# Performance work log

Hardware: AMD Instinct MI355X
Metric: run time of the kernel (lower is better)

The kernel has to match this reference:

```python
import jax, jax.numpy as jnp
import numpy as np

B, S, E, H = 4, 2048, 1024, 16
DH = E // H  # 64
DF = 4 * E   # 4096
EPS = 1e-5


def layer_norm(x, g, b):
    mu = jnp.mean(x, axis=-1, keepdims=True)
    var = jnp.mean(jnp.square(x - mu), axis=-1, keepdims=True)
    return (x - mu) * jax.lax.rsqrt(var + EPS) * g + b


def setup_inputs() -> dict:
    key = jax.random.key(0)
    ks = jax.random.split(key, 16)
    s_e = 1.0 / np.sqrt(E)
    s_f = 1.0 / np.sqrt(DF)
    inp = {
        "x": jax.random.normal(ks[0], (B, S, E), jnp.float32),
        # per-head projections stacked over heads: [H, E, DH]
        "wq": jax.random.normal(ks[1], (H, E, DH), jnp.float32) * s_e,
        "wk": jax.random.normal(ks[2], (H, E, DH), jnp.float32) * s_e,
        "wv": jax.random.normal(ks[3], (H, E, DH), jnp.float32) * s_e,
        # output projection [H*DH, E] with bias
        "wo": jax.random.normal(ks[4], (H * DH, E), jnp.float32) * s_e,
        "bo": jax.random.normal(ks[5], (E,), jnp.float32) * 0.01,
        # SwiGLU FFN
        "w1": jax.random.normal(ks[6], (E, DF), jnp.float32) * s_e,
        "b1": jax.random.normal(ks[7], (DF,), jnp.float32) * 0.01,
        "w2": jax.random.normal(ks[8], (E, DF), jnp.float32) * s_e,
        "b2": jax.random.normal(ks[9], (DF,), jnp.float32) * 0.01,
        "w3": jax.random.normal(ks[10], (DF, E), jnp.float32) * s_f,
        "b3": jax.random.normal(ks[11], (E,), jnp.float32) * 0.01,
        # LayerNorm params
        "g1": jnp.ones((E,), jnp.float32),
        "be1": jnp.zeros((E,), jnp.float32),
        "g2": jnp.ones((E,), jnp.float32),
        "be2": jnp.zeros((E,), jnp.float32),
    }
    return inp


def reference(x, wq, wk, wv, wo, bo, w1, b1, w2, b2, w3, b3, g1, be1, g2, be2):
    # --- LN1 + multi-head causal attention ---
    h = layer_norm(x, g1, be1)                       # [B,S,E]
    q = jnp.einsum('bse,hed->bhsd', h, wq)           # [B,H,S,DH]
    k = jnp.einsum('bse,hed->bhsd', h, wk)
    v = jnp.einsum('bse,hed->bhsd', h, wv)
    scores = jnp.einsum('bhsd,bhtd->bhst', q, k) * (DH ** -0.5)  # [B,H,S,S]
    causal = jnp.tril(jnp.ones((S, S), bool))
    scores = jnp.where(causal, scores, -jnp.inf)
    attn = jax.nn.softmax(scores, axis=-1)
    ctx = jnp.einsum('bhst,bhtd->bhsd', attn, v)     # [B,H,S,DH]
    ctx = ctx.transpose(0, 2, 1, 3).reshape(B, S, H * DH)  # concat heads
    attn_out = ctx @ wo + bo                         # [B,S,E]
    r1 = x + attn_out
    # --- LN2 + SwiGLU FFN ---
    h2 = layer_norm(r1, g2, be2)
    a = h2 @ w1 + b1                                 # [B,S,DF]
    gate = h2 @ w2 + b2
    ff = (a * jax.nn.sigmoid(a) * gate) @ w3 + b3    # [B,S,E]
    return r1 + ff
```

## Files before the change

kernel.cpp:

```cpp
#include <hip/hip_runtime.h>
#include <hip/hip_bf16.h>
#include <cstdint>


typedef __bf16 bf16_t;
typedef __attribute__((ext_vector_type(8))) __bf16 bf16x8;
typedef __attribute__((ext_vector_type(4))) __bf16 bf16x4;
typedef __attribute__((ext_vector_type(4))) float f32x4;

#define LOG2E 1.4426950408889634f

static __device__ __forceinline__ void gll16(const void* g, void* l) {
  __builtin_amdgcn_global_load_lds(
      (const __attribute__((address_space(1))) void*)g,
      (__attribute__((address_space(3))) void*)l, 16, 0, 0);
}

template<int PACK>
__global__ __launch_bounds__(256)
void transpose_cvt(const float* __restrict__ in, bf16_t* __restrict__ out,
                   int R, int C, long in_batch, long out_batch, int off)
{
  __shared__ float tile[64][65];
  const float* inp = in + (long)blockIdx.z * in_batch;
  bf16_t* outp = out + (long)blockIdx.z * out_batch;
  const int c0 = blockIdx.x * 64, r0 = blockIdx.y * 64;
  for (int rr = threadIdx.y; rr < 64; rr += 4)
    tile[rr][threadIdx.x] = inp[(long)(r0 + rr) * C + c0 + threadIdx.x];
  __syncthreads();
  for (int cc = threadIdx.y; cc < 64; cc += 4) {
    const int c = c0 + cc;
    const long orow = PACK ? (long)((c >> 4) * 32 + (c & 15) + off) : (long)c;
    outp[orow * R + r0 + threadIdx.x] = (bf16_t)tile[threadIdx.x][cc];
  }
}

template<int BF16IN>
__global__ __launch_bounds__(256)
void ln_kernel(const void* __restrict__ xin, const float* __restrict__ g,
               const float* __restrict__ be, bf16_t* __restrict__ out)
{
  const long row = blockIdx.x;
  float e0, e1, e2, e3;
  if constexpr (BF16IN) {
    const bf16x4 v = ((const bf16x4*)((const bf16_t*)xin + row * 1024))[threadIdx.x];
    e0 = (float)v[0]; e1 = (float)v[1]; e2 = (float)v[2]; e3 = (float)v[3];
  } else {
    const float4 v = ((const float4*)((const float*)xin + row * 1024))[threadIdx.x];
    e0 = v.x; e1 = v.y; e2 = v.z; e3 = v.w;
  }
  float s  = e0 + e1 + e2 + e3;
  float s2 = e0*e0 + e1*e1 + e2*e2 + e3*e3;
  #pragma unroll
  for (int m = 1; m < 64; m <<= 1) {
    s  += __shfl_xor(s, m, 64);
    s2 += __shfl_xor(s2, m, 64);
  }
  __shared__ float red[8];
  const int w = threadIdx.x >> 6, lane = threadIdx.x & 63;
  if (lane == 0) { red[w] = s; red[4 + w] = s2; }
  __syncthreads();
  s  = red[0] + red[1] + red[2] + red[3];
  s2 = red[4] + red[5] + red[6] + red[7];
  const float mu = s * (1.f / 1024.f);
  const float rs = rsqrtf(s2 * (1.f / 1024.f) - mu * mu + 1e-5f);
  const int c = threadIdx.x * 4;
  bf16x4 o;
  o[0] = (bf16_t)((e0 - mu) * rs * g[c+0] + be[c+0]);
  o[1] = (bf16_t)((e1 - mu) * rs * g[c+1] + be[c+1]);
  o[2] = (bf16_t)((e2 - mu) * rs * g[c+2] + be[c+2]);
  o[3] = (bf16_t)((e3 - mu) * rs * g[c+3] + be[c+3]);
  *(bf16x4*)(out + row * 1024 + c) = o;
}

template<int EPI, int KT>
__global__ __launch_bounds__(256)
void gemm16(const bf16_t* __restrict__ A, const bf16_t* __restrict__ Bt,
            const float* __restrict__ bias, const float* __restrict__ bias2,
            const float* __restrict__ resF, const bf16_t* __restrict__ resB,
            float* __restrict__ outF, bf16_t* __restrict__ outB,
            bf16_t* __restrict__ outQ, bf16_t* __restrict__ outK, bf16_t* __restrict__ outV,
            int N)
{
  __shared__ __align__(16) bf16_t As[2][128 * 32];
  __shared__ __align__(16) bf16_t Bs[2][128 * 32];
  const int tid = threadIdx.x, lane = tid & 63, w = tid >> 6;
  const int wr = w >> 1, wc = w & 1;
  const long row0 = (long)blockIdx.y * 128;
  const long col0 = (long)blockIdx.x * 128;
  const int rsub = lane >> 2;
  const int csub = (lane & 3) * 8;
  const int kof = (lane >> 4) * 8;
  f32x4 acc[4][4] = {};

  auto stage = [&](long k0, int buf) {
    #pragma unroll
    for (int i = 0; i < 2; ++i) {
      const int c = i * 4 + w;
      gll16(A  + (row0 + c * 16 + rsub) * (long)KT + k0 + csub, (char*)As[buf] + c * 1024);
      gll16(Bt + (col0 + c * 16 + rsub) * (long)KT + k0 + csub, (char*)Bs[buf] + c * 1024);
    }
  };

  stage(0, 0);
  __syncthreads();
  int cur = 0;
  for (long k0 = 0; k0 < KT; k0 += 32) {
    if (k0 + 32 < KT) stage(k0 + 32, cur ^ 1);
    bf16x8 af[4], bfr[4];
    #pragma unroll
    for (int m = 0; m < 4; ++m)
      af[m] = *(const bf16x8*)(As[cur] + (wr * 64 + m * 16 + (lane & 15)) * 32 + kof);
    #pragma unroll
    for (int n = 0; n < 4; ++n)
      bfr[n] = *(const bf16x8*)(Bs[cur] + (wc * 64 + n * 16 + (lane & 15)) * 32 + kof);
    #pragma unroll
    for (int m = 0; m < 4; ++m)
      #pragma unroll
      for (int n = 0; n < 4; ++n)
        acc[m][n] = __builtin_amdgcn_mfma_f32_16x16x32_bf16(af[m], bfr[n], acc[m][n], 0, 0, 0);
    __syncthreads();
    cur ^= 1;
  }

  if constexpr (EPI == 3) {
    const long L0 = ((col0 + wc * 64) >> 5) * 16;
    #pragma unroll
    for (int m = 0; m < 4; ++m) {
      #pragma unroll
      for (int np = 0; np < 2; ++np) {
        const long lc = L0 + np * 16 + (lane & 15);
        #pragma unroll
        for (int r = 0; r < 4; ++r) {
          const long rr = row0 + wr * 64 + m * 16 + (lane >> 4) * 4 + r;
          const float a  = acc[m][2 * np][r] + bias[lc];
          const float gt = acc[m][2 * np + 1][r] + bias2[lc];
          const float sig = 1.0f / (1.0f + __expf(-a));
          outB[rr * N + lc] = (bf16_t)(a * sig * gt);
        }
      }
    }
  } else {
    #pragma unroll
    for (int m = 0; m < 4; ++m) {
      #pragma unroll
      for (int n = 0; n < 4; ++n) {
        const long cc = col0 + wc * 64 + n * 16 + (lane & 15);
        #pragma unroll
        for (int r = 0; r < 4; ++r) {
          const long rr = row0 + wr * 64 + m * 16 + (lane >> 4) * 4 + r;
          const float v = acc[m][n][r];
          if constexpr (EPI == 0) {
            const int which = (int)(cc >> 10);
            const int hh = (int)((cc >> 6) & 15);
            const int d  = (int)(cc & 63);
            const long b = rr >> 11, s2 = rr & 2047;
            const bf16_t bv = (bf16_t)v;
            const long bh = b * 16 + hh;
            if (which == 0)      outQ[(bh * 2048 + s2) * 64 + d] = bv;
            else if (which == 1) outK[(bh * 2048 + s2) * 64 + d] = bv;
            else                 outV[(bh * 64 + d) * 2048 + s2] = bv;
          } else if constexpr (EPI == 1) {
            outB[rr * N + cc] = (bf16_t)(v + bias[cc] + resF[rr * N + cc]);
          } else {
            outF[rr * N + cc] = v + bias[cc] + (float)resB[rr * N + cc];
          }
        }
      }
    }
  }
}

__global__ __launch_bounds__(256, 4)
void attn_kernel(const bf16_t* __restrict__ q, const bf16_t* __restrict__ k,
                 const bf16_t* __restrict__ vT, bf16_t* __restrict__ ctx)
{
  __shared__ __align__(16) bf16_t Kb[2][64 * 64];
  __shared__ __align__(16) bf16_t Vb[2][64 * 64];
  __shared__ __align__(16) bf16_t plds[4][16 * 64];
  const int tid = threadIdx.x, lane = tid & 63, wvi = tid >> 6;
  const int bh = blockIdx.x;
  const bf16_t* qp = q  + (long)bh * 2048 * 64;
  const bf16_t* kp = k  + (long)bh * 2048 * 64;
  const bf16_t* vp = vT + (long)bh * 64 * 2048;
  const int l15 = lane & 15, lhi = lane >> 4;
  const long b = bh >> 4;
  const int hh = bh & 15;
  const int sw = (l15 & 7);
  const int psw = sw << 1;

  const int r0s = tid >> 3, cp0 = tid & 7, cl0 = cp0 ^ (r0s & 7);
  const int r1s = (tid + 256) >> 3, cp1 = tid & 7, cl1 = cp1 ^ (r1s & 7);

  #pragma unroll
  for (int seg = 0; seg < 2; ++seg) {
    const int ts = (seg == 0) ? blockIdx.y : 31 - blockIdx.y;
    const int qw0 = ts * 64 + wvi * 16;
    const int q_glob = qw0 + l15;
    bf16x8 qf[2];
    #pragma unroll
    for (int kk = 0; kk < 2; ++kk)
      qf[kk] = *(const bf16x8*)(qp + (long)(qw0 + l15) * 64 + kk * 32 + lhi * 8);
    f32x4 accO[4] = {};
    float mrow = -1e30f, lrow = 0.f;

    gll16(kp + (long)(0 + r0s) * 64 + cl0 * 8, (char*)Kb[0] + tid * 16);
    gll16(vp + (long)r0s * 2048 + 0 + cl0 * 8, (char*)Vb[0] + tid * 16);
    gll16(kp + (long)(0 + r1s) * 64 + cl1 * 8, (char*)Kb[0] + (tid + 256) * 16);
    gll16(vp + (long)r1s * 2048 + 0 + cl1 * 8, (char*)Vb[0] + (tid + 256) * 16);
    __syncthreads();

    int cur = 0;
    const int kbmax = ts * 64;
    for (int kb = 0; kb <= kbmax; kb += 64) {
      if (kb + 64 <= kbmax) {
        const int nb = kb + 64;
        gll16(kp + (long)(nb + r0s) * 64 + cl0 * 8, (char*)Kb[cur ^ 1] + tid * 16);
        gll16(vp + (long)r0s * 2048 + nb + cl0 * 8, (char*)Vb[cur ^ 1] + tid * 16);
        gll16(kp + (long)(nb + r1s) * 64 + cl1 * 8, (char*)Kb[cur ^ 1] + (tid + 256) * 16);
        gll16(vp + (long)r1s * 2048 + nb + cl1 * 8, (char*)Vb[cur ^ 1] + (tid + 256) * 16);
      }
      f32x4 accS[4] = {};
      #pragma unroll
      for (int n = 0; n < 4; ++n) {
        const bf16_t* kr = Kb[cur] + (n * 16 + l15) * 64;
        #pragma unroll
        for (int kk = 0; kk < 2; ++kk) {
          const bf16x8 kf = *(const bf16x8*)(kr + ((kk * 4 + lhi) ^ sw) * 8);
          accS[n] = __builtin_amdgcn_mfma_f32_16x16x32_bf16(kf, qf[kk], accS[n], 0, 0, 0);
        }
      }
      const bool needmask = (kb + 63 > qw0);
      float rmax = -1e30f;
      #pragma unroll
      for (int n = 0; n < 4; ++n)
        #pragma unroll
        for (int r = 0; r < 4; ++r) {
          float sv = accS[n][r] * 0.125f;
          if (needmask && (kb + n * 16 + lhi * 4 + r > q_glob)) sv = -1e30f;
          accS[n][r] = sv;
          rmax = fmaxf(rmax, sv);
        }
      rmax = fmaxf(rmax, __shfl_xor(rmax, 16, 64));
      rmax = fmaxf(rmax, __shfl_xor(rmax, 32, 64));
      const float mn = fmaxf(mrow, rmax);
      const float corr = exp2f((mrow - mn) * LOG2E);
      mrow = mn;
      float rsum = 0.f;
      #pragma unroll
      for (int n = 0; n < 4; ++n)
        #pragma unroll
        for (int r = 0; r < 4; ++r) {
          const float p = exp2f((accS[n][r] - mn) * LOG2E);
          accS[n][r] = p;
          rsum += p;
        }
      rsum += __shfl_xor(rsum, 16, 64);
      rsum += __shfl_xor(rsum, 32, 64);
      lrow = lrow * corr + rsum;
      #pragma unroll
      for (int nd = 0; nd < 4; ++nd)
        #pragma unroll
        for (int r = 0; r < 4; ++r) accO[nd][r] *= corr;
      #pragma unroll
      for (int n = 0; n < 4; ++n) {
        bf16x4 pk;
        #pragma unroll
        for (int r = 0; r < 4; ++r) pk[r] = (bf16_t)accS[n][r];
        *(bf16x4*)(&plds[wvi][l15 * 64 + ((4 * n + lhi) ^ psw) * 4]) = pk;
      }
      #pragma unroll
      for (int kk = 0; kk < 2; ++kk) {
        const bf16x8 pf = *(const bf16x8*)(&plds[wvi][l15 * 64 + ((8 * kk + 2 * lhi) ^ psw) * 4]);
        #pragma unroll
        for (int nd = 0; nd < 4; ++nd) {
          const bf16x8 vf = *(const bf16x8*)(Vb[cur] + (nd * 16 + l15) * 64 + ((kk * 4 + lhi) ^ sw) * 8);
          accO[nd] = __builtin_amdgcn_mfma_f32_16x16x32_bf16(vf, pf, accO[nd], 0, 0, 0);
        }
      }
      __syncthreads();
      cur ^= 1;
    }
    const float inv = 1.f / lrow;
    const long crow = (b * 2048 + qw0 + l15) * 1024 + hh * 64;
    #pragma unroll
    for (int nd = 0; nd < 4; ++nd) {
      bf16x4 ok;
      #pragma unroll
      for (int r = 0; r < 4; ++r) ok[r] = (bf16_t)(accO[nd][r] * inv);
      *(bf16x4*)(ctx + crow + nd * 16 + lhi * 4) = ok;
    }
  }
}

extern "C" void kernel_launch(void* const* d_in, const int* in_sizes, int n_in,
                              void* d_out, int out_size, void* d_ws, size_t ws_size,
                              hipStream_t stream)
{
  const float* x   = (const float*)d_in[0];
  const float* wq  = (const float*)d_in[1];
  const float* wk  = (const float*)d_in[2];
  const float* wv  = (const float*)d_in[3];
  const float* wo  = (const float*)d_in[4];
  const float* bo  = (const float*)d_in[5];
  const float* w1  = (const float*)d_in[6];
  const float* b1  = (const float*)d_in[7];
  const float* w2  = (const float*)d_in[8];
  const float* b2  = (const float*)d_in[9];
  const float* w3  = (const float*)d_in[10];
  const float* b3  = (const float*)d_in[11];
  const float* g1  = (const float*)d_in[12];
  const float* be1 = (const float*)d_in[13];
  const float* g2  = (const float*)d_in[14];
  const float* be2 = (const float*)d_in[15];
  float* out = (float*)d_out;

  char* ws = (char*)d_ws;
  bf16_t* h    = (bf16_t*)(ws);
  bf16_t* qb   = (bf16_t*)(ws + 16777216L);
  bf16_t* kb   = (bf16_t*)(ws + 2 * 16777216L);
  bf16_t* vTb  = (bf16_t*)(ws + 3 * 16777216L);
  bf16_t* r1b  = (bf16_t*)(ws + 4 * 16777216L);
  bf16_t* ffin = (bf16_t*)(ws + 4 * 16777216L + 33554432L);
  char* wbase  = ws + 4 * 16777216L + 33554432L + 67108864L;
  bf16_t* Wqkvt = (bf16_t*)(wbase);
  bf16_t* Wot   = (bf16_t*)(wbase + 6291456L);
  bf16_t* Wp    = (bf16_t*)(wbase + 8388608L);
  bf16_t* W3t   = (bf16_t*)(wbase + 25165824L);

  const dim3 tb(64, 4);
  transpose_cvt<0><<<dim3(1, 16, 16), tb, 0, stream>>>(wq, Wqkvt,            1024, 64, 65536, 65536, 0);
  transpose_cvt<0><<<dim3(1, 16, 16), tb, 0, stream>>>(wk, Wqkvt + 1048576L, 1024, 64, 65536, 65536, 0);
  transpose_cvt<0><<<dim3(1, 16, 16), tb, 0, stream>>>(wv, Wqkvt + 2097152L, 1024, 64, 65536, 65536, 0);
  transpose_cvt<0><<<dim3(16, 16, 1), tb, 0, stream>>>(wo, Wot, 1024, 1024, 0, 0, 0);
  transpose_cvt<1><<<dim3(64, 16, 1), tb, 0, stream>>>(w1, Wp, 1024, 4096, 0, 0, 0);
  transpose_cvt<1><<<dim3(64, 16, 1), tb, 0, stream>>>(w2, Wp, 1024, 4096, 0, 0, 16);
  transpose_cvt<0><<<dim3(16, 64, 1), tb, 0, stream>>>(w3, W3t, 4096, 1024, 0, 0, 0);
  ln_kernel<0><<<8192, 256, 0, stream>>>(x, g1, be1, h);
  gemm16<0, 1024><<<dim3(24, 64), 256, 0, stream>>>(h, Wqkvt, nullptr, nullptr, nullptr, nullptr,
                                                    nullptr, nullptr, qb, kb, vTb, 3072);
  attn_kernel<<<dim3(64, 16), 256, 0, stream>>>(qb, kb, vTb, h);
  gemm16<1, 1024><<<dim3(8, 64), 256, 0, stream>>>(h, Wot, bo, nullptr, x, nullptr,
                                                   nullptr, r1b, nullptr, nullptr, nullptr, 1024);
  ln_kernel<1><<<8192, 256, 0, stream>>>(r1b, g2, be2, qb);
  gemm16<3, 1024><<<dim3(64, 64), 256, 0, stream>>>(qb, Wp, b1, b2, nullptr, nullptr,
                                                    nullptr, ffin, nullptr, nullptr, nullptr, 4096);
  gemm16<2, 4096><<<dim3(8, 64), 256, 0, stream>>>(ffin, W3t, b3, nullptr, nullptr, r1b,
                                                   out, nullptr, nullptr, nullptr, nullptr, 1024);
}
```

Baseline: 542.6 us.

## Add 256x256-tile 8-wave GEMM for QKV and SwiGLU FFN projections

Adds a new GEMM kernel with 256x256 output tiles, 512 threads, 64-wide K tiles, XOR-swizzled LDS layout, and a hand-scheduled pipeline. The pipeline interleaves global-to-LDS staging with MFMA phases using explicit barriers, sched_barrier and setprio. It replaces the 128x128 gemm16 for the QKV projection and the fused W1/W2 SwiGLU GEMM to raise arithmetic intensity per LDS byte and cut global reloads. The trade-offs are higher register and LDS pressure (128 KB LDS per block, so occupancy is limited) and fewer blocks for the QKV GEMM (384), which may not fill all CUs evenly.

After: 564.7 us. 1.04x slower.

```diff
diff --git a/kernel.cpp b/kernel.cpp
--- a/kernel.cpp
+++ b/kernel.cpp
@@ -73,14 +73,147 @@
   *(bf16x4*)(out + row * 1024 + c) = o;
 }
 
+template<int EPI>
+__global__ __launch_bounds__(512, 2)
+void gemm256(const bf16_t* __restrict__ A, const bf16_t* __restrict__ Bt,
+             const float* __restrict__ bias, const float* __restrict__ bias2,
+             bf16_t* __restrict__ outB,
+             bf16_t* __restrict__ outQ, bf16_t* __restrict__ outK, bf16_t* __restrict__ outV,
+             int N)
+{
+  __shared__ __align__(16) bf16_t Asl[2][2][128 * 64];
+  __shared__ __align__(16) bf16_t Bsl[2][2][128 * 64];
+  constexpr int KT = 1024;
+  constexpr int NT = KT / 64;
+  const int tid = threadIdx.x, lane = tid & 63;
+  const int w = tid >> 6, wr = w >> 2, wc = w & 3;
+  const long row0 = (long)blockIdx.y * 256;
+  const long col0 = (long)blockIdx.x * 256;
+  const int l15 = lane & 15, lhi = lane >> 4;
+  const int offk0 = ((lhi ^ (l15 & 7)) & 7) * 8;
+  const int r1 = tid >> 3;
+  const int c1 = (tid & 7) ^ (r1 & 7);
+  f32x4 acc[8][4] = {};
+
+  auto stageA = [&](int t, int buf) {
+    const long kb = (long)t * 64 + c1 * 8;
+    #pragma unroll
+    for (int h = 0; h < 2; ++h) {
+      gll16(A + (row0 + h * 128 + r1) * (long)KT + kb,      (char*)Asl[buf][h] + tid * 16);
+      gll16(A + (row0 + h * 128 + r1 + 64) * (long)KT + kb, (char*)Asl[buf][h] + (tid + 512) * 16);
+    }
+  };
+  auto stageB = [&](int t, int buf) {
+    const long kb = (long)t * 64 + c1 * 8;
+    #pragma unroll
+    for (int h = 0; h < 2; ++h) {
+      gll16(Bt + (col0 + h * 128 + r1) * (long)KT + kb,      (char*)Bsl[buf][h] + tid * 16);
+      gll16(Bt + (col0 + h * 128 + r1 + 64) * (long)KT + kb, (char*)Bsl[buf][h] + (tid + 512) * 16);
+    }
+  };
+
+  auto ktile = [&](int t, int rb, int wb) {
+    const bf16_t* Ah = Asl[rb][wr];
+    const bf16_t* Bb = Bsl[rb][wc >> 1] + (wc & 1) * 64 * 64;
+    const bool dostage = (t + 1 < NT);
+    #pragma unroll
+    for (int p = 0; p < 4; ++p) {
+      const int mh = p >> 1, nh = p & 1;
+      bf16x8 af[4][2], bfr[2][2];
+      const bf16_t* ap = Ah + (mh * 64 + l15) * 64;
+      #pragma unroll
+      for (int m = 0; m < 4; ++m) {
+        af[m][0] = *(const bf16x8*)(ap + m * 16 * 64 + offk0);
+        af[m][1] = *(const bf16x8*)(ap + m * 16 * 64 + (offk0 ^ 32));
+      }
+      const bf16_t* bp = Bb + (nh * 32 + l15) * 64;
+      #pragma unroll
+      for (int n = 0; n < 2; ++n) {
+        bfr[n][0] = *(const bf16x8*)(bp + n * 16 * 64 + offk0);
+        bfr[n][1] = *(const bf16x8*)(bp + n * 16 * 64 + (offk0 ^ 32));
+      }
+      if (dostage) {
+        if (p == 0) stageA(t + 1, wb);
+        if (p == 1) stageB(t + 1, wb);
+      }
+      __builtin_amdgcn_sched_barrier(0);
+      __builtin_amdgcn_s_barrier();
+      __builtin_amdgcn_sched_barrier(0);
+      __builtin_amdgcn_s_setprio(1);
+      #pragma unroll
+      for (int m = 0; m < 4; ++m)
+        #pragma unroll
+        for (int n = 0; n < 2; ++n)
+          #pragma unroll
+          for (int ks = 0; ks < 2; ++ks)
+            acc[mh * 4 + m][nh * 2 + n] = __builtin_amdgcn_mfma_f32_16x16x32_bf16(
+                af[m][ks], bfr[n][ks], acc[mh * 4 + m][nh * 2 + n], 0, 0, 0);
+      __builtin_amdgcn_s_setprio(0);
+      __builtin_amdgcn_sched_barrier(0);
+      if (p == 3) asm volatile("s_waitcnt vmcnt(0)" ::: "memory");
+      __builtin_amdgcn_s_barrier();
+      __builtin_amdgcn_sched_barrier(0);
+    }
+  };
+
+  stageA(0, 0);
+  stageB(0, 0);
+  asm volatile("s_waitcnt vmcnt(0)" ::: "memory");
+  __builtin_amdgcn_s_barrier();
+  __builtin_amdgcn_sched_barrier(0);
+
+  for (int tt = 0; tt < NT; tt += 2) {
+    ktile(tt, 0, 1);
+    ktile(tt + 1, 1, 0);
+  }
+
+  if constexpr (EPI == 3) {
+    const long L0 = ((col0 + wc * 64) >> 5) * 16;
+    #pragma unroll
+    for (int M = 0; M < 8; ++M) {
+      #pragma unroll
+      for (int np = 0; np < 2; ++np) {
+        const long lc = L0 + np * 16 + l15;
+        #pragma unroll
+        for (int r = 0; r < 4; ++r) {
+          const long rr = row0 + wr * 128 + M * 16 + lhi * 4 + r;
+          const float a  = acc[M][2 * np][r] + bias[lc];
+          const float gt = acc[M][2 * np + 1][r] + bias2[lc];
+          const float sig = 1.0f / (1.0f + __expf(-a));
+          outB[rr * N + lc] = (bf16_t)(a * sig * gt);
+        }
+      }
+    }
+  } else {
+    #pragma unroll
+    for (int M = 0; M < 8; ++M) {
+      #pragma unroll
+      for (int n = 0; n < 4; ++n) {
+        const long cc = col0 + wc * 64 + n * 16 + l15;
+        #pragma unroll
+        for (int r = 0; r < 4; ++r) {
+          const long rr = row0 + wr * 128 + M * 16 + lhi * 4 + r;
+          const bf16_t bv = (bf16_t)acc[M][n][r];
+          const int which = (int)(cc >> 10);
+          const int hh = (int)((cc >> 6) & 15);
+          const int d  = (int)(cc & 63);
+          const long b = rr >> 11, s2 = rr & 2047;
+          const long bh = b * 16 + hh;
+          if (which == 0)      outQ[(bh * 2048 + s2) * 64 + d] = bv;
+          else if (which == 1) outK[(bh * 2048 + s2) * 64 + d] = bv;
+          else                 outV[(bh * 64 + d) * 2048 + s2] = bv;
+        }
+      }
+    }
+  }
+}
+
 template<int EPI, int KT>
 __global__ __launch_bounds__(256)
 void gemm16(const bf16_t* __restrict__ A, const bf16_t* __restrict__ Bt,
-            const float* __restrict__ bias, const float* __restrict__ bias2,
+            const float* __restrict__ bias,
             const float* __restrict__ resF, const bf16_t* __restrict__ resB,
-            float* __restrict__ outF, bf16_t* __restrict__ outB,
-            bf16_t* __restrict__ outQ, bf16_t* __restrict__ outK, bf16_t* __restrict__ outV,
-            int N)
+            float* __restrict__ outF, bf16_t* __restrict__ outB, int N)
 {
   __shared__ __align__(16) bf16_t As[2][128 * 32];
   __shared__ __align__(16) bf16_t Bs[2][128 * 32];
@@ -122,49 +255,19 @@
     __syncthreads();
     cur ^= 1;
   }
-
-  if constexpr (EPI == 3) {
-    const long L0 = ((col0 + wc * 64) >> 5) * 16;
-    #pragma unroll
-    for (int m = 0; m < 4; ++m) {
-      #pragma unroll
-      for (int np = 0; np < 2; ++np) {
-        const long lc = L0 + np * 16 + (lane & 15);
-        #pragma unroll
-        for (int r = 0; r < 4; ++r) {
-          const long rr = row0 + wr * 64 + m * 16 + (lane >> 4) * 4 + r;
-          const float a  = acc[m][2 * np][r] + bias[lc];
-          const float gt = acc[m][2 * np + 1][r] + bias2[lc];
-          const float sig = 1.0f / (1.0f + __expf(-a));
-          outB[rr * N + lc] = (bf16_t)(a * sig * gt);
-        }
-      }
-    }
-  } else {
-    #pragma unroll
-    for (int m = 0; m < 4; ++m) {
-      #pragma unroll
-      for (int n = 0; n < 4; ++n) {
-        const long cc = col0 + wc * 64 + n * 16 + (lane & 15);
-        #pragma unroll
-        for (int r = 0; r < 4; ++r) {
-          const long rr = row0 + wr * 64 + m * 16 + (lane >> 4) * 4 + r;
-          const float v = acc[m][n][r];
-          if constexpr (EPI == 0) {
-            const int which = (int)(cc >> 10);
-            const int hh = (int)((cc >> 6) & 15);
-            const int d  = (int)(cc & 63);
-            const long b = rr >> 11, s2 = rr & 2047;
-            const bf16_t bv = (bf16_t)v;
-            const long bh = b * 16 + hh;
-            if (which == 0)      outQ[(bh * 2048 + s2) * 64 + d] = bv;
-            else if (which == 1) outK[(bh * 2048 + s2) * 64 + d] = bv;
-            else                 outV[(bh * 64 + d) * 2048 + s2] = bv;
-          } else if constexpr (EPI == 1) {
-            outB[rr * N + cc] = (bf16_t)(v + bias[cc] + resF[rr * N + cc]);
-          } else {
-            outF[rr * N + cc] = v + bias[cc] + (float)resB[rr * N + cc];
-          }
+  #pragma unroll
+  for (int m = 0; m < 4; ++m) {
+    #pragma unroll
+    for (int n = 0; n < 4; ++n) {
+      const long cc = col0 + wc * 64 + n * 16 + (lane & 15);
+      #pragma unroll
+      for (int r = 0; r < 4; ++r) {
+        const long rr = row0 + wr * 64 + m * 16 + (lane >> 4) * 4 + r;
+        const float v = acc[m][n][r];
+        if constexpr (EPI == 1) {
+          outB[rr * N + cc] = (bf16_t)(v + bias[cc] + resF[rr * N + cc]);
+        } else {
+          outF[rr * N + cc] = v + bias[cc] + (float)resB[rr * N + cc];
         }
       }
     }
@@ -189,8 +292,8 @@
   const int sw = (l15 & 7);
   const int psw = sw << 1;
 
-  const int r0s = tid >> 3, cp0 = tid & 7, cl0 = cp0 ^ (r0s & 7);
-  const int r1s = (tid + 256) >> 3, cp1 = tid & 7, cl1 = cp1 ^ (r1s & 7);
+  const int r0s = tid >> 3, cl0 = (tid & 7) ^ (r0s & 7);
+  const int r1s = (tid + 256) >> 3, cl1 = (tid & 7) ^ (r1s & 7);
 
   #pragma unroll
   for (int seg = 0; seg < 2; ++seg) {
@@ -337,14 +440,14 @@
   transpose_cvt<1><<<dim3(64, 16, 1), tb, 0, stream>>>(w2, Wp, 1024, 4096, 0, 0, 16);
   transpose_cvt<0><<<dim3(16, 64, 1), tb, 0, stream>>>(w3, W3t, 4096, 1024, 0, 0, 0);
   ln_kernel<0><<<8192, 256, 0, stream>>>(x, g1, be1, h);
-  gemm16<0, 1024><<<dim3(24, 64), 256, 0, stream>>>(h, Wqkvt, nullptr, nullptr, nullptr, nullptr,
-                                                    nullptr, nullptr, qb, kb, vTb, 3072);
+  gemm256<0><<<dim3(12, 32), 512, 0, stream>>>(h, Wqkvt, nullptr, nullptr,
+                                               nullptr, qb, kb, vTb, 3072);
   attn_kernel<<<dim3(64, 16), 256, 0, stream>>>(qb, kb, vTb, h);
-  gemm16<1, 1024><<<dim3(8, 64), 256, 0, stream>>>(h, Wot, bo, nullptr, x, nullptr,
-                                                   nullptr, r1b, nullptr, nullptr, nullptr, 1024);
+  gemm16<1, 1024><<<dim3(8, 64), 256, 0, stream>>>(h, Wot, bo, x, nullptr,
+                                                   nullptr, r1b, 1024);
   ln_kernel<1><<<8192, 256, 0, stream>>>(r1b, g2, be2, qb);
-  gemm16<3, 1024><<<dim3(64, 64), 256, 0, stream>>>(qb, Wp, b1, b2, nullptr, nullptr,
-                                                    nullptr, ffin, nullptr, nullptr, nullptr, 4096);
-  gemm16<2, 4096><<<dim3(8, 64), 256, 0, stream>>>(ffin, W3t, b3, nullptr, nullptr, r1b,
-                                                   out, nullptr, nullptr, nullptr, nullptr, 1024);
-}
+  gemm256<3><<<dim3(32, 32), 512, 0, stream>>>(qb, Wp, b1, b2,
+                                               ffin, nullptr, nullptr, nullptr, 4096);
+  gemm16<2, 4096><<<dim3(8, 64), 256, 0, stream>>>(ffin, W3t, b3, nullptr, r1b,
+                                                   out, nullptr, 1024);
+}
```

## Enlarge GEMM tiles to 256x128 with XOR-swizzled LDS and MFMA priority

Applied to the files above, without the earlier changes.

Replaces the 128x128 GEMM tile with a 256x128 tile, giving each wave 8x4 MFMA accumulators. This raises arithmetic intensity and halves the grid rows. It also changes LDS staging to a row-major layout with an XOR swizzle on the 16-byte chunk index to avoid bank conflicts, and raises wave priority around the MFMA block. The costs are doubled accumulator registers (launch bounds set to 2 blocks per CU), more LDS per block, and fewer blocks for the small N=1024 GEMMs (256 blocks).

Result: slower. 577.8 us (+6.5%).

```diff
diff --git a/kernel.cpp b/kernel.cpp
--- a/kernel.cpp
+++ b/kernel.cpp
@@ -74,31 +74,33 @@
 }
 
 template<int EPI, int KT>
-__global__ __launch_bounds__(256)
-void gemm16(const bf16_t* __restrict__ A, const bf16_t* __restrict__ Bt,
-            const float* __restrict__ bias, const float* __restrict__ bias2,
-            const float* __restrict__ resF, const bf16_t* __restrict__ resB,
-            float* __restrict__ outF, bf16_t* __restrict__ outB,
-            bf16_t* __restrict__ outQ, bf16_t* __restrict__ outK, bf16_t* __restrict__ outV,
-            int N)
-{
-  __shared__ __align__(16) bf16_t As[2][128 * 32];
+__global__ __launch_bounds__(256, 2)
+void gemmW(const bf16_t* __restrict__ A, const bf16_t* __restrict__ Bt,
+           const float* __restrict__ bias, const float* __restrict__ bias2,
+           const float* __restrict__ resF, const bf16_t* __restrict__ resB,
+           float* __restrict__ outF, bf16_t* __restrict__ outB,
+           bf16_t* __restrict__ outQ, bf16_t* __restrict__ outK, bf16_t* __restrict__ outV,
+           int N)
+{
+  __shared__ __align__(16) bf16_t As[2][256 * 32];
   __shared__ __align__(16) bf16_t Bs[2][128 * 32];
   const int tid = threadIdx.x, lane = tid & 63, w = tid >> 6;
   const int wr = w >> 1, wc = w & 1;
-  const long row0 = (long)blockIdx.y * 128;
+  const long row0 = (long)blockIdx.y * 256;
   const long col0 = (long)blockIdx.x * 128;
-  const int rsub = lane >> 2;
-  const int csub = (lane & 3) * 8;
-  const int kof = (lane >> 4) * 8;
-  f32x4 acc[4][4] = {};
+  const int l15 = lane & 15, lhi = lane >> 4;
+  f32x4 acc[8][4] = {};
 
   auto stage = [&](long k0, int buf) {
     #pragma unroll
+    for (int i = 0; i < 4; ++i) {
+      const int p = tid + 256 * i, rA = p >> 2, cA = (p & 3) ^ (rA & 3);
+      gll16(A + (row0 + rA) * (long)KT + k0 + cA * 8, (char*)As[buf] + p * 16);
+    }
+    #pragma unroll
     for (int i = 0; i < 2; ++i) {
-      const int c = i * 4 + w;
-      gll16(A  + (row0 + c * 16 + rsub) * (long)KT + k0 + csub, (char*)As[buf] + c * 1024);
-      gll16(Bt + (col0 + c * 16 + rsub) * (long)KT + k0 + csub, (char*)Bs[buf] + c * 1024);
+      const int p = tid + 256 * i, rB = p >> 2, cB = (p & 3) ^ (rB & 3);
+      gll16(Bt + (col0 + rB) * (long)KT + k0 + cB * 8, (char*)Bs[buf] + p * 16);
     }
   };
 
@@ -107,18 +109,25 @@
   int cur = 0;
   for (long k0 = 0; k0 < KT; k0 += 32) {
     if (k0 + 32 < KT) stage(k0 + 32, cur ^ 1);
-    bf16x8 af[4], bfr[4];
-    #pragma unroll
-    for (int m = 0; m < 4; ++m)
-      af[m] = *(const bf16x8*)(As[cur] + (wr * 64 + m * 16 + (lane & 15)) * 32 + kof);
-    #pragma unroll
-    for (int n = 0; n < 4; ++n)
-      bfr[n] = *(const bf16x8*)(Bs[cur] + (wc * 64 + n * 16 + (lane & 15)) * 32 + kof);
-    #pragma unroll
-    for (int m = 0; m < 4; ++m)
+    bf16x8 bfr[4];
+    #pragma unroll
+    for (int n = 0; n < 4; ++n) {
+      const int row = wc * 64 + n * 16 + l15;
+      bfr[n] = *(const bf16x8*)(Bs[cur] + row * 32 + (lhi ^ (row & 3)) * 8);
+    }
+    bf16x8 af[8];
+    #pragma unroll
+    for (int m = 0; m < 8; ++m) {
+      const int row = wr * 128 + m * 16 + l15;
+      af[m] = *(const bf16x8*)(As[cur] + row * 32 + (lhi ^ (row & 3)) * 8);
+    }
+    __builtin_amdgcn_s_setprio(1);
+    #pragma unroll
+    for (int m = 0; m < 8; ++m)
       #pragma unroll
       for (int n = 0; n < 4; ++n)
         acc[m][n] = __builtin_amdgcn_mfma_f32_16x16x32_bf16(af[m], bfr[n], acc[m][n], 0, 0, 0);
+    __builtin_amdgcn_s_setprio(0);
     __syncthreads();
     cur ^= 1;
   }
@@ -126,13 +135,13 @@
   if constexpr (EPI == 3) {
     const long L0 = ((col0 + wc * 64) >> 5) * 16;
     #pragma unroll
-    for (int m = 0; m < 4; ++m) {
+    for (int m = 0; m < 8; ++m) {
       #pragma unroll
       for (int np = 0; np < 2; ++np) {
-        const long lc = L0 + np * 16 + (lane & 15);
+        const long lc = L0 + np * 16 + l15;
         #pragma unroll
         for (int r = 0; r < 4; ++r) {
-          const long rr = row0 + wr * 64 + m * 16 + (lane >> 4) * 4 + r;
+          const long rr = row0 + wr * 128 + m * 16 + lhi * 4 + r;
           const float a  = acc[m][2 * np][r] + bias[lc];
           const float gt = acc[m][2 * np + 1][r] + bias2[lc];
           const float sig = 1.0f / (1.0f + __expf(-a));
@@ -142,13 +151,13 @@
     }
   } else {
     #pragma unroll
-    for (int m = 0; m < 4; ++m) {
+    for (int m = 0; m < 8; ++m) {
       #pragma unroll
       for (int n = 0; n < 4; ++n) {
-        const long cc = col0 + wc * 64 + n * 16 + (lane & 15);
+        const long cc = col0 + wc * 64 + n * 16 + l15;
         #pragma unroll
         for (int r = 0; r < 4; ++r) {
-          const long rr = row0 + wr * 64 + m * 16 + (lane >> 4) * 4 + r;
+          const long rr = row0 + wr * 128 + m * 16 + lhi * 4 + r;
           const float v = acc[m][n][r];
           if constexpr (EPI == 0) {
             const int which = (int)(cc >> 10);
@@ -189,8 +198,8 @@
   const int sw = (l15 & 7);
   const int psw = sw << 1;
 
-  const int r0s = tid >> 3, cp0 = tid & 7, cl0 = cp0 ^ (r0s & 7);
-  const int r1s = (tid + 256) >> 3, cp1 = tid & 7, cl1 = cp1 ^ (r1s & 7);
+  const int r0s = tid >> 3, cl0 = (tid & 7) ^ (r0s & 7);
+  const int r1s = (tid + 256) >> 3, cl1 = (tid & 7) ^ (r1s & 7);
 
   #pragma unroll
   for (int seg = 0; seg < 2; ++seg) {
@@ -337,14 +346,14 @@
   transpose_cvt<1><<<dim3(64, 16, 1), tb, 0, stream>>>(w2, Wp, 1024, 4096, 0, 0, 16);
   transpose_cvt<0><<<dim3(16, 64, 1), tb, 0, stream>>>(w3, W3t, 4096, 1024, 0, 0, 0);
   ln_kernel<0><<<8192, 256, 0, stream>>>(x, g1, be1, h);
-  gemm16<0, 1024><<<dim3(24, 64), 256, 0, stream>>>(h, Wqkvt, nullptr, nullptr, nullptr, nullptr,
-                                                    nullptr, nullptr, qb, kb, vTb, 3072);
+  gemmW<0, 1024><<<dim3(24, 32), 256, 0, stream>>>(h, Wqkvt, nullptr, nullptr, nullptr, nullptr,
+                                                   nullptr, nullptr, qb, kb, vTb, 3072);
   attn_kernel<<<dim3(64, 16), 256, 0, stream>>>(qb, kb, vTb, h);
-  gemm16<1, 1024><<<dim3(8, 64), 256, 0, stream>>>(h, Wot, bo, nullptr, x, nullptr,
-                                                   nullptr, r1b, nullptr, nullptr, nullptr, 1024);
+  gemmW<1, 1024><<<dim3(8, 32), 256, 0, stream>>>(h, Wot, bo, nullptr, x, nullptr,
+                                                  nullptr, r1b, nullptr, nullptr, nullptr, 1024);
   ln_kernel<1><<<8192, 256, 0, stream>>>(r1b, g2, be2, qb);
-  gemm16<3, 1024><<<dim3(64, 64), 256, 0, stream>>>(qb, Wp, b1, b2, nullptr, nullptr,
-                                                    nullptr, ffin, nullptr, nullptr, nullptr, 4096);
-  gemm16<2, 4096><<<dim3(8, 64), 256, 0, stream>>>(ffin, W3t, b3, nullptr, nullptr, r1b,
-                                                   out, nullptr, nullptr, nullptr, nullptr, 1024);
-}
+  gemmW<3, 1024><<<dim3(64, 32), 256, 0, stream>>>(qb, Wp, b1, b2, nullptr, nullptr,
+                                                   nullptr, ffin, nullptr, nullptr, nullptr, 4096);
+  gemmW<2, 4096><<<dim3(8, 32), 256, 0, stream>>>(ffin, W3t, b3, nullptr, nullptr, r1b,
+                                                  out, nullptr, nullptr, nullptr, nullptr, 1024);
+}
```
